# Optimization experiments

Hardware: AMD Instinct MI355X
Metric: run time of the kernel (lower is better)

Reference implementation:

```python
import jax, jax.numpy as jnp
import numpy as np

RANK = 16
ALPHA = 32
SCALING = ALPHA / RANK  # 2.0


def setup_inputs() -> dict:
    key = jax.random.key(0)
    k1, k2, k3 = jax.random.split(key, 3)
    B_, S, D, O = 2, 4096, 4096, 4096
    x = jax.random.normal(k1, (B_, S, D), dtype=jnp.float32)
    # Dequantized base weight, torch Linear layout [out, in]
    W_base = jax.random.normal(k2, (O, D), dtype=jnp.float32) * 0.02
    # kaiming_uniform-ish init for lora_A [rank, in]
    bound = float(np.sqrt(6.0 / (1 + 5) / D))
    A = jax.random.uniform(k3, (RANK, D), dtype=jnp.float32, minval=-bound, maxval=bound)
    # lora_B initialized to zeros [out, rank]
    Bm = jnp.zeros((O, RANK), dtype=jnp.float32)
    return {"x": x, "W_base": W_base, "A": A, "B": Bm}


def reference(x, W_base, A, B):
    # Y = x @ W_base^T + (x @ A^T) @ B^T * scaling   (dropout p=0 -> identity)
    base_out = jnp.einsum('bsd,od->bso', x, W_base)
    lora_mid = jnp.einsum('bsd,rd->bsr', x, A)        # [B,S,rank]
    lora_out = jnp.einsum('bsr,or->bso', lora_mid, B) # [B,S,out]
    return base_out + lora_out * SCALING
```

## Files before the change

kernel.cpp:

```cpp
#include <hip/hip_runtime.h>
#include <hip/hip_bf16.h>

typedef __attribute__((ext_vector_type(8)))  __bf16 bf16x8;
typedef __attribute__((ext_vector_type(4)))  float  f32x4;

__global__ __launch_bounds__(256) void preproc(
    const float* __restrict__ x, const float* __restrict__ A,
    const float* __restrict__ Wf,
    float* __restrict__ mid, __bf16* __restrict__ Xb, __bf16* __restrict__ Wbb,
    int K, int M, long nW8, int wBlocks)
{
    int tid = threadIdx.x;
    if ((int)blockIdx.x < wBlocks) {
        long i = (long)blockIdx.x * 256 + tid;
        long stride = (long)wBlocks * 256;
        for (; i < nW8; i += stride) {
            const f32x4* p = (const f32x4*)(Wf + i * 8);
            f32x4 a = p[0], b = p[1];
            bf16x8 o;
            o[0] = (__bf16)a[0]; o[1] = (__bf16)a[1];
            o[2] = (__bf16)a[2]; o[3] = (__bf16)a[3];
            o[4] = (__bf16)b[0]; o[5] = (__bf16)b[1];
            o[6] = (__bf16)b[2]; o[7] = (__bf16)b[3];
            *(bf16x8*)(Wbb + i * 8) = o;
        }
        return;
    }

    int m0 = ((int)blockIdx.x - wBlocks) * 4;
    float acc[4][16];
#pragma unroll
    for (int row = 0; row < 4; ++row)
#pragma unroll
        for (int r = 0; r < 16; ++r) acc[row][r] = 0.f;

    int iters = K / 2048;
    for (int it = 0; it < iters; ++it) {
        int k = it * 2048 + tid * 8;
        f32x4 xv[4][2];
#pragma unroll
        for (int row = 0; row < 4; ++row) {
            if (m0 + row < M) {
                const float* xr = x + (size_t)(m0 + row) * K;
                xv[row][0] = *(const f32x4*)(xr + k);
                xv[row][1] = *(const f32x4*)(xr + k + 4);
                bf16x8 o;
                o[0] = (__bf16)xv[row][0][0]; o[1] = (__bf16)xv[row][0][1];
                o[2] = (__bf16)xv[row][0][2]; o[3] = (__bf16)xv[row][0][3];
                o[4] = (__bf16)xv[row][1][0]; o[5] = (__bf16)xv[row][1][1];
                o[6] = (__bf16)xv[row][1][2]; o[7] = (__bf16)xv[row][1][3];
                *(bf16x8*)(Xb + (size_t)(m0 + row) * K + k) = o;
            } else {
                f32x4 z = {0.f,0.f,0.f,0.f};
                xv[row][0] = z; xv[row][1] = z;
            }
        }
#pragma unroll
        for (int r = 0; r < 16; ++r) {
            const f32x4* ap = (const f32x4*)(A + (size_t)r * K + k);
            f32x4 a0 = ap[0], a1 = ap[1];
#pragma unroll
            for (int row = 0; row < 4; ++row) {
                acc[row][r] += xv[row][0][0]*a0[0] + xv[row][0][1]*a0[1]
                             + xv[row][0][2]*a0[2] + xv[row][0][3]*a0[3]
                             + xv[row][1][0]*a1[0] + xv[row][1][1]*a1[1]
                             + xv[row][1][2]*a1[2] + xv[row][1][3]*a1[3];
            }
        }
    }

#pragma unroll
    for (int row = 0; row < 4; ++row)
#pragma unroll
        for (int r = 0; r < 16; ++r)
#pragma unroll
            for (int off = 32; off > 0; off >>= 1)
                acc[row][r] += __shfl_down(acc[row][r], off, 64);

    __shared__ float red[4][4][16];
    int lane = tid & 63, w = tid >> 6;
    if (lane == 0) {
#pragma unroll
        for (int row = 0; row < 4; ++row)
#pragma unroll
            for (int r = 0; r < 16; ++r) red[w][row][r] = acc[row][r];
    }
    __syncthreads();
    if (tid < 64) {
        int row = tid >> 4, r = tid & 15;
        if (m0 + row < M) {
            float s = red[0][row][r] + red[1][row][r]
                    + red[2][row][r] + red[3][row][r];
            mid[(size_t)(m0 + row) * 16 + r] = s;
        }
    }
}

__global__ __launch_bounds__(256) void mid_only(
    const float* __restrict__ x, const float* __restrict__ A,
    float* __restrict__ mid, int K, int M)
{
    int tid = threadIdx.x;
    int m0 = blockIdx.x * 4;
    float acc[4][16];
#pragma unroll
    for (int row = 0; row < 4; ++row)
#pragma unroll
        for (int r = 0; r < 16; ++r) acc[row][r] = 0.f;
    int iters = K / 2048;
    for (int it = 0; it < iters; ++it) {
        int k = it * 2048 + tid * 8;
        f32x4 xv[4][2];
#pragma unroll
        for (int row = 0; row < 4; ++row) {
            if (m0 + row < M) {
                const float* xr = x + (size_t)(m0 + row) * K;
                xv[row][0] = *(const f32x4*)(xr + k);
                xv[row][1] = *(const f32x4*)(xr + k + 4);
            } else {
                f32x4 z = {0.f,0.f,0.f,0.f};
                xv[row][0] = z; xv[row][1] = z;
            }
        }
#pragma unroll
        for (int r = 0; r < 16; ++r) {
            const f32x4* ap = (const f32x4*)(A + (size_t)r * K + k);
            f32x4 a0 = ap[0], a1 = ap[1];
#pragma unroll
            for (int row = 0; row < 4; ++row) {
                acc[row][r] += xv[row][0][0]*a0[0] + xv[row][0][1]*a0[1]
                             + xv[row][0][2]*a0[2] + xv[row][0][3]*a0[3]
                             + xv[row][1][0]*a1[0] + xv[row][1][1]*a1[1]
                             + xv[row][1][2]*a1[2] + xv[row][1][3]*a1[3];
            }
        }
    }
#pragma unroll
    for (int row = 0; row < 4; ++row)
#pragma unroll
        for (int r = 0; r < 16; ++r)
#pragma unroll
            for (int off = 32; off > 0; off >>= 1)
                acc[row][r] += __shfl_down(acc[row][r], off, 64);
    __shared__ float red[4][4][16];
    int lane = tid & 63, w = tid >> 6;
    if (lane == 0) {
#pragma unroll
        for (int row = 0; row < 4; ++row)
#pragma unroll
            for (int r = 0; r < 16; ++r) red[w][row][r] = acc[row][r];
    }
    __syncthreads();
    if (tid < 64) {
        int row = tid >> 4, r = tid & 15;
        if (m0 + row < M) {
            float s = red[0][row][r] + red[1][row][r]
                    + red[2][row][r] + red[3][row][r];
            mid[(size_t)(m0 + row) * 16 + r] = s;
        }
    }
}

#define GL16(g, l) __builtin_amdgcn_global_load_lds( \
    (const __attribute__((address_space(1))) void*)(g), \
    (__attribute__((address_space(3))) void*)(l), 16, 0, 0)

#define DSR(dst, addr, IMM) \
    asm volatile("ds_read_b128 %0, %1 offset:" IMM : "=v"(dst) : "v"(addr))

#define BAR()   __builtin_amdgcn_s_barrier()
#define LGKM0() asm volatile("s_waitcnt lgkmcnt(0)" ::: )
#define SCHED() __builtin_amdgcn_sched_barrier(0)
#define VMW(n)  asm volatile("s_waitcnt vmcnt(" #n ")" ::: "memory")

__global__ __launch_bounds__(512, 2) void gemm256(
    const __bf16* __restrict__ Xb,
    const __bf16* __restrict__ Wb,
    const float*  __restrict__ mid,
    const float*  __restrict__ Bl,
    float* __restrict__ out,
    int M, int N, int K)
{
    __shared__ __bf16 As[4][256 * 32];
    __shared__ __bf16 Bs[4][256 * 32];

    const int NT = K >> 5;

    int nbx = N >> 8, nby = M >> 8, nwg = nbx * nby;
    int bid = blockIdx.x, swz = bid;
    if ((nwg & 7) == 0) { int cpx = nwg >> 3; swz = (bid & 7) * cpx + (bid >> 3); }
    int by = swz / nbx, bx = swz % nbx;
    int m0 = by << 8, n0 = bx << 8;

    int tid = threadIdx.x;
    int lane = tid & 63;
    int w = tid >> 6;
    int wm = w >> 2, wn = w & 3;

    int q0 = tid >> 2;
    int c0 = tid & 3;
    int csrc = c0 ^ ((q0 >> 1) & 3);
    const __bf16* sA0 = Xb + (size_t)(m0 + q0) * K + csrc * 8;
    const __bf16* sA1 = sA0 + (size_t)128 * K;
    const __bf16* sB0 = Wb + (size_t)(n0 + q0) * K + csrc * 8;
    const __bf16* sB1 = sB0 + (size_t)128 * K;
    unsigned ldsw = (unsigned)w * 1024;

#define STAGE_A(t, b) do { size_t ko = (size_t)(t) * 32; \
    GL16(sA0 + ko, (char*)As[b] + ldsw); \
    GL16(sA1 + ko, (char*)As[b] + 8192 + ldsw); } while (0)
#define STAGE_B(t, b) do { size_t ko = (size_t)(t) * 32; \
    GL16(sB0 + ko, (char*)Bs[b] + ldsw); \
    GL16(sB1 + ko, (char*)Bs[b] + 8192 + ldsw); } while (0)

    int chunkSwz = (lane >> 4) ^ ((lane >> 1) & 3);
    unsigned aoff = (unsigned)((wm * 128 + (lane & 15)) * 64 + chunkSwz * 16);
    unsigned boff = (unsigned)((wn * 64  + (lane & 15)) * 64 + chunkSwz * 16);
    unsigned a_addr = (unsigned)(size_t)(__attribute__((address_space(3))) __bf16*)&As[0][0] + aoff;
    unsigned b_addr = (unsigned)(size_t)(__attribute__((address_space(3))) __bf16*)&Bs[0][0] + boff;

    f32x4 acc[8][4];
    {
        int kh = lane >> 4;
        bf16x8 bI[4];
#pragma unroll
        for (int j = 0; j < 4; ++j) {
            bf16x8 v = {};
            if (kh < 2) {
                int col = n0 + wn * 64 + j * 16 + (lane & 15);
                const f32x4* p = (const f32x4*)(Bl + (size_t)col * 16 + kh * 8);
                f32x4 v0 = p[0], v1 = p[1];
                v[0] = (__bf16)(2.0f * v0[0]); v[1] = (__bf16)(2.0f * v0[1]);
                v[2] = (__bf16)(2.0f * v0[2]); v[3] = (__bf16)(2.0f * v0[3]);
                v[4] = (__bf16)(2.0f * v1[0]); v[5] = (__bf16)(2.0f * v1[1]);
                v[6] = (__bf16)(2.0f * v1[2]); v[7] = (__bf16)(2.0f * v1[3]);
            }
            bI[j] = v;
        }
#pragma unroll
        for (int i = 0; i < 8; ++i) {
            bf16x8 aI = {};
            if (kh < 2) {
                int row = m0 + wm * 128 + i * 16 + (lane & 15);
                const f32x4* p = (const f32x4*)(mid + (size_t)row * 16 + kh * 8);
                f32x4 v0 = p[0], v1 = p[1];
                aI[0] = (__bf16)v0[0]; aI[1] = (__bf16)v0[1];
                aI[2] = (__bf16)v0[2]; aI[3] = (__bf16)v0[3];
                aI[4] = (__bf16)v1[0]; aI[5] = (__bf16)v1[1];
                aI[6] = (__bf16)v1[2]; aI[7] = (__bf16)v1[3];
            }
            f32x4 z = {0.f, 0.f, 0.f, 0.f};
#pragma unroll
            for (int j = 0; j < 4; ++j)
                acc[i][j] = __builtin_amdgcn_mfma_f32_16x16x32_bf16(aI, bI[j], z, 0, 0, 0);
        }
    }

    STAGE_A(0, 0); STAGE_B(0, 0);
    STAGE_A(1, 1); STAGE_B(1, 1);
    STAGE_A(2, 2); STAGE_B(2, 2);
    STAGE_A(3, 3); STAGE_B(3, 3);
    VMW(12);
    BAR();

    bf16x8 axf0, axf1, axf2, axf3, bxf0, bxf1, bxf2, bxf3;
    bf16x8 ayf0, ayf1, ayf2, ayf3, byf0, byf1, byf2, byf3;
    bf16x8 ax4, ax5, ax6, ax7, ay4, ay5, ay6, ay7;

    DSR(axf0, a_addr, "0");    DSR(axf1, a_addr, "1024");
    DSR(axf2, a_addr, "2048"); DSR(axf3, a_addr, "3072");
    DSR(bxf0, b_addr, "0");    DSR(bxf1, b_addr, "1024");
    DSR(bxf2, b_addr, "2048"); DSR(bxf3, b_addr, "3072");

    for (int t = 0; t < NT; t += 2) {
        unsigned aT0 = a_addr + ((unsigned)(t & 3) << 14);
        unsigned aT1 = a_addr + ((unsigned)((t + 1) & 3) << 14);
        unsigned bT1 = b_addr + ((unsigned)((t + 1) & 3) << 14);
        unsigned aT2 = a_addr + ((unsigned)((t + 2) & 3) << 14);
        unsigned bT2 = b_addr + ((unsigned)((t + 2) & 3) << 14);
        bool p2 = (t + 2) < NT;
        bool p3 = (t + 3) < NT;
        bool p4 = (t + 4) < NT;
        bool p5 = (t + 5) < NT;

        LGKM0();
        BAR();
        SCHED();
        DSR(ax4, aT0, "4096"); DSR(ax5, aT0, "5120");
        DSR(ax6, aT0, "6144"); DSR(ax7, aT0, "7168");
        SCHED();
        __builtin_amdgcn_s_setprio(1);
        acc[0][0] = __builtin_amdgcn_mfma_f32_16x16x32_bf16(axf0, bxf0, acc[0][0], 0, 0, 0);
        acc[0][1] = __builtin_amdgcn_mfma_f32_16x16x32_bf16(axf0, bxf1, acc[0][1], 0, 0, 0);
        acc[0][2] = __builtin_amdgcn_mfma_f32_16x16x32_bf16(axf0, bxf2, acc[0][2], 0, 0, 0);
        acc[0][3] = __builtin_amdgcn_mfma_f32_16x16x32_bf16(axf0, bxf3, acc[0][3], 0, 0, 0);
        acc[1][0] = __builtin_amdgcn_mfma_f32_16x16x32_bf16(axf1, bxf0, acc[1][0], 0, 0, 0);
        acc[1][1] = __builtin_amdgcn_mfma_f32_16x16x32_bf16(axf1, bxf1, acc[1][1], 0, 0, 0);
        acc[1][2] = __builtin_amdgcn_mfma_f32_16x16x32_bf16(axf1, bxf2, acc[1][2], 0, 0, 0);
        acc[1][3] = __builtin_amdgcn_mfma_f32_16x16x32_bf16(axf1, bxf3, acc[1][3], 0, 0, 0);
        acc[2][0] = __builtin_amdgcn_mfma_f32_16x16x32_bf16(axf2, bxf0, acc[2][0], 0, 0, 0);
        acc[2][1] = __builtin_amdgcn_mfma_f32_16x16x32_bf16(axf2, bxf1, acc[2][1], 0, 0, 0);
        acc[2][2] = __builtin_amdgcn_mfma_f32_16x16x32_bf16(axf2, bxf2, acc[2][2], 0, 0, 0);
        acc[2][3] = __builtin_amdgcn_mfma_f32_16x16x32_bf16(axf2, bxf3, acc[2][3], 0, 0, 0);
        acc[3][0] = __builtin_amdgcn_mfma_f32_16x16x32_bf16(axf3, bxf0, acc[3][0], 0, 0, 0);
        acc[3][1] = __builtin_amdgcn_mfma_f32_16x16x32_bf16(axf3, bxf1, acc[3][1], 0, 0, 0);
        acc[3][2] = __builtin_amdgcn_mfma_f32_16x16x32_bf16(axf3, bxf2, acc[3][2], 0, 0, 0);
        acc[3][3] = __builtin_amdgcn_mfma_f32_16x16x32_bf16(axf3, bxf3, acc[3][3], 0, 0, 0);
        __builtin_amdgcn_s_setprio(0);

        LGKM0();
        if (p3)      { VMW(8); }
        else if (p2) { VMW(4); }
        else         { VMW(0); }
        BAR();
        SCHED();
        DSR(ayf0, aT1, "0");    DSR(ayf1, aT1, "1024");
        DSR(ayf2, aT1, "2048"); DSR(ayf3, aT1, "3072");
        DSR(byf0, bT1, "0");    DSR(byf1, bT1, "1024");
        DSR(byf2, bT1, "2048"); DSR(byf3, bT1, "3072");
        if (p4) { STAGE_A(t + 4, t & 3); STAGE_B(t + 4, t & 3); }
        SCHED();
        __builtin_amdgcn_s_setprio(1);
        acc[4][0] = __builtin_amdgcn_mfma_f32_16x16x32_bf16(ax4, bxf0, acc[4][0], 0, 0, 0);
        acc[4][1] = __builtin_amdgcn_mfma_f32_16x16x32_bf16(ax4, bxf1, acc[4][1], 0, 0, 0);
        acc[4][2] = __builtin_amdgcn_mfma_f32_16x16x32_bf16(ax4, bxf2, acc[4][2], 0, 0, 0);
        acc[4][3] = __builtin_amdgcn_mfma_f32_16x16x32_bf16(ax4, bxf3, acc[4][3], 0, 0, 0);
        acc[5][0] = __builtin_amdgcn_mfma_f32_16x16x32_bf16(ax5, bxf0, acc[5][0], 0, 0, 0);
        acc[5][1] = __builtin_amdgcn_mfma_f32_16x16x32_bf16(ax5, bxf1, acc[5][1], 0, 0, 0);
        acc[5][2] = __builtin_amdgcn_mfma_f32_16x16x32_bf16(ax5, bxf2, acc[5][2], 0, 0, 0);
        acc[5][3] = __builtin_amdgcn_mfma_f32_16x16x32_bf16(ax5, bxf3, acc[5][3], 0, 0, 0);
        acc[6][0] = __builtin_amdgcn_mfma_f32_16x16x32_bf16(ax6, bxf0, acc[6][0], 0, 0, 0);
        acc[6][1] = __builtin_amdgcn_mfma_f32_16x16x32_bf16(ax6, bxf1, acc[6][1], 0, 0, 0);
        acc[6][2] = __builtin_amdgcn_mfma_f32_16x16x32_bf16(ax6, bxf2, acc[6][2], 0, 0, 0);
        acc[6][3] = __builtin_amdgcn_mfma_f32_16x16x32_bf16(ax6, bxf3, acc[6][3], 0, 0, 0);
        acc[7][0] = __builtin_amdgcn_mfma_f32_16x16x32_bf16(ax7, bxf0, acc[7][0], 0, 0, 0);
        acc[7][1] = __builtin_amdgcn_mfma_f32_16x16x32_bf16(ax7, bxf1, acc[7][1], 0, 0, 0);
        acc[7][2] = __builtin_amdgcn_mfma_f32_16x16x32_bf16(ax7, bxf2, acc[7][2], 0, 0, 0);
        acc[7][3] = __builtin_amdgcn_mfma_f32_16x16x32_bf16(ax7, bxf3, acc[7][3], 0, 0, 0);
        __builtin_amdgcn_s_setprio(0);

        LGKM0();
        BAR();
        SCHED();
        DSR(ay4, aT1, "4096"); DSR(ay5, aT1, "5120");
        DSR(ay6, aT1, "6144"); DSR(ay7, aT1, "7168");
        SCHED();
        __builtin_amdgcn_s_setprio(1);
        acc[0][0] = __builtin_amdgcn_mfma_f32_16x16x32_bf16(ayf0, byf0, acc[0][0], 0, 0, 0);
        acc[0][1] = __builtin_amdgcn_mfma_f32_16x16x32_bf16(ayf0, byf1, acc[0][1], 0, 0, 0);
        acc[0][2] = __builtin_amdgcn_mfma_f32_16x16x32_bf16(ayf0, byf2, acc[0][2], 0, 0, 0);
        acc[0][3] = __builtin_amdgcn_mfma_f32_16x16x32_bf16(ayf0, byf3, acc[0][3], 0, 0, 0);
        acc[1][0] = __builtin_amdgcn_mfma_f32_16x16x32_bf16(ayf1, byf0, acc[1][0], 0, 0, 0);
        acc[1][1] = __builtin_amdgcn_mfma_f32_16x16x32_bf16(ayf1, byf1, acc[1][1], 0, 0, 0);
        acc[1][2] = __builtin_amdgcn_mfma_f32_16x16x32_bf16(ayf1, byf2, acc[1][2], 0, 0, 0);
        acc[1][3] = __builtin_amdgcn_mfma_f32_16x16x32_bf16(ayf1, byf3, acc[1][3], 0, 0, 0);
        acc[2][0] = __builtin_amdgcn_mfma_f32_16x16x32_bf16(ayf2, byf0, acc[2][0], 0, 0, 0);
        acc[2][1] = __builtin_amdgcn_mfma_f32_16x16x32_bf16(ayf2, byf1, acc[2][1], 0, 0, 0);
        acc[2][2] = __builtin_amdgcn_mfma_f32_16x16x32_bf16(ayf2, byf2, acc[2][2], 0, 0, 0);
        acc[2][3] = __builtin_amdgcn_mfma_f32_16x16x32_bf16(ayf2, byf3, acc[2][3], 0, 0, 0);
        acc[3][0] = __builtin_amdgcn_mfma_f32_16x16x32_bf16(ayf3, byf0, acc[3][0], 0, 0, 0);
        acc[3][1] = __builtin_amdgcn_mfma_f32_16x16x32_bf16(ayf3, byf1, acc[3][1], 0, 0, 0);
        acc[3][2] = __builtin_amdgcn_mfma_f32_16x16x32_bf16(ayf3, byf2, acc[3][2], 0, 0, 0);
        acc[3][3] = __builtin_amdgcn_mfma_f32_16x16x32_bf16(ayf3, byf3, acc[3][3], 0, 0, 0);
        __builtin_amdgcn_s_setprio(0);

        LGKM0();
        if (p4)      { VMW(8); }
        else if (p3) { VMW(4); }
        else         { VMW(0); }
        BAR();
        SCHED();
        if (p2) {
            DSR(axf0, aT2, "0");    DSR(axf1, aT2, "1024");
            DSR(axf2, aT2, "2048"); DSR(axf3, aT2, "3072");
            DSR(bxf0, bT2, "0");    DSR(bxf1, bT2, "1024");
            DSR(bxf2, bT2, "2048"); DSR(bxf3, bT2, "3072");
        }
        if (p5) { STAGE_A(t + 5, (t + 1) & 3); STAGE_B(t + 5, (t + 1) & 3); }
        SCHED();
        __builtin_amdgcn_s_setprio(1);
        acc[4][0] = __builtin_amdgcn_mfma_f32_16x16x32_bf16(ay4, byf0, acc[4][0], 0, 0, 0);
        acc[4][1] = __builtin_amdgcn_mfma_f32_16x16x32_bf16(ay4, byf1, acc[4][1], 0, 0, 0);
        acc[4][2] = __builtin_amdgcn_mfma_f32_16x16x32_bf16(ay4, byf2, acc[4][2], 0, 0, 0);
        acc[4][3] = __builtin_amdgcn_mfma_f32_16x16x32_bf16(ay4, byf3, acc[4][3], 0, 0, 0);
        acc[5][0] = __builtin_amdgcn_mfma_f32_16x16x32_bf16(ay5, byf0, acc[5][0], 0, 0, 0);
        acc[5][1] = __builtin_amdgcn_mfma_f32_16x16x32_bf16(ay5, byf1, acc[5][1], 0, 0, 0);
        acc[5][2] = __builtin_amdgcn_mfma_f32_16x16x32_bf16(ay5, byf2, acc[5][2], 0, 0, 0);
        acc[5][3] = __builtin_amdgcn_mfma_f32_16x16x32_bf16(ay5, byf3, acc[5][3], 0, 0, 0);
        acc[6][0] = __builtin_amdgcn_mfma_f32_16x16x32_bf16(ay6, byf0, acc[6][0], 0, 0, 0);
        acc[6][1] = __builtin_amdgcn_mfma_f32_16x16x32_bf16(ay6, byf1, acc[6][1], 0, 0, 0);
        acc[6][2] = __builtin_amdgcn_mfma_f32_16x16x32_bf16(ay6, byf2, acc[6][2], 0, 0, 0);
        acc[6][3] = __builtin_amdgcn_mfma_f32_16x16x32_bf16(ay6, byf3, acc[6][3], 0, 0, 0);
        acc[7][0] = __builtin_amdgcn_mfma_f32_16x16x32_bf16(ay7, byf0, acc[7][0], 0, 0, 0);
        acc[7][1] = __builtin_amdgcn_mfma_f32_16x16x32_bf16(ay7, byf1, acc[7][1], 0, 0, 0);
        acc[7][2] = __builtin_amdgcn_mfma_f32_16x16x32_bf16(ay7, byf2, acc[7][2], 0, 0, 0);
        acc[7][3] = __builtin_amdgcn_mfma_f32_16x16x32_bf16(ay7, byf3, acc[7][3], 0, 0, 0);
        __builtin_amdgcn_s_setprio(0);
    }

#pragma unroll
    for (int i = 0; i < 8; ++i) {
        int rbase = m0 + wm * 128 + i * 16 + ((lane >> 4) << 2);
#pragma unroll
        for (int q = 0; q < 4; ++q) {
            float* orow = out + (size_t)(rbase + q) * N;
            int colb = n0 + wn * 64 + (lane & 15);
            orow[colb]      = acc[i][0][q];
            orow[colb + 16] = acc[i][1][q];
            orow[colb + 32] = acc[i][2][q];
            orow[colb + 48] = acc[i][3][q];
        }
    }
}

__global__ __launch_bounds__(256) void gemm_fb(
    const float* __restrict__ X, const float* __restrict__ W,
    const float* __restrict__ mid, const float* __restrict__ Bl,
    float* __restrict__ out, int M, int N, int K)
{
    __shared__ float As[64][16];
    __shared__ float Bs[64][16];
    int nbx = N / 64;
    int bx = blockIdx.x % nbx, by = blockIdx.x / nbx;
    int m0 = by * 64, n0 = bx * 64;
    int tid = threadIdx.x;
    int tr = tid >> 4, tc = tid & 15;

    float acc[4][4] = {};
    for (int kt = 0; kt < K; kt += 16) {
#pragma unroll
        for (int s = 0; s < 4; ++s) {
            int c = s * 256 + tid;
            int row = c >> 4, kk = c & 15;
            As[row][kk] = X[(size_t)(m0 + row) * K + kt + kk];
            Bs[row][kk] = W[(size_t)(n0 + row) * K + kt + kk];
        }
        __syncthreads();
#pragma unroll
        for (int kk = 0; kk < 16; ++kk) {
            float av[4], bv[4];
#pragma unroll
            for (int i = 0; i < 4; ++i) { av[i] = As[tr*4+i][kk]; bv[i] = Bs[tc*4+i][kk]; }
#pragma unroll
            for (int i = 0; i < 4; ++i)
#pragma unroll
                for (int j = 0; j < 4; ++j) acc[i][j] += av[i] * bv[j];
        }
        __syncthreads();
    }
#pragma unroll
    for (int i = 0; i < 4; ++i) {
        int row = m0 + tr * 4 + i;
#pragma unroll
        for (int j = 0; j < 4; ++j) {
            int col = n0 + tc * 4 + j;
            float s = 0.f;
#pragma unroll
            for (int r = 0; r < 16; ++r)
                s += mid[(size_t)row * 16 + r] * Bl[(size_t)col * 16 + r];
            out[(size_t)row * N + col] = acc[i][j] + 2.0f * s;
        }
    }
}

extern "C" void kernel_launch(void* const* d_in, const int* in_sizes, int n_in,
                              void* d_out, int out_size, void* d_ws, size_t ws_size,
                              hipStream_t stream)
{
    const float* x   = (const float*)d_in[0];
    const float* Wf  = (const float*)d_in[1];
    const float* A   = (const float*)d_in[2];
    const float* Bl  = (const float*)d_in[3];
    float* out = (float*)d_out;

    int D = in_sizes[2] / 16;
    int O = in_sizes[3] / 16;
    long M = (long)in_sizes[0] / D;
    int K = D, N = O;

    size_t xb_bytes  = (size_t)M * K * 2;
    size_t wb_bytes  = (size_t)N * K * 2;
    size_t mid_bytes = (size_t)M * 16 * 4;

    bool shapes_ok = (M % 256 == 0) && (N % 256 == 0) && (K % 2048 == 0)
                     && (K / 32 >= 8);

    int midBlocks = (int)((M + 3) / 4);

    if (shapes_ok && ws_size >= xb_bytes + wb_bytes + mid_bytes) {
        __bf16* Xb  = (__bf16*)d_ws;
        __bf16* Wbb = (__bf16*)((char*)d_ws + xb_bytes);
        float*  mid = (float*)((char*)d_ws + xb_bytes + wb_bytes);

        const int wBlocks = 1024;
        long nW8 = (long)N * K / 8;
        preproc<<<wBlocks + midBlocks, 256, 0, stream>>>(
            x, A, Wf, mid, Xb, Wbb, K, (int)M, nW8, wBlocks);
        int nwg = (int)(M / 256) * (N / 256);
        gemm256<<<nwg, 512, 0, stream>>>(Xb, Wbb, mid, Bl, out, (int)M, N, K);
    } else {
        float* mid = (float*)d_ws;
        mid_only<<<midBlocks, 256, 0, stream>>>(x, A, mid, K, (int)M);
        int nwg = (int)(M / 64) * (N / 64);
        gemm_fb<<<nwg, 256, 0, stream>>>(x, Wf, mid, Bl, out, (int)M, N, K);
    }
}
```

Before: 330.6 us.

## Restructure GEMM main loop to two-stage prefetch with split A/B staging

Replaces the 4-deep global-to-LDS prefetch and register double-buffered fragment loads with a simpler per-tile loop. It prefetches only 2 tiles ahead and issues the A stage and B stage in separate halves of the iteration. LDS fragment reads are no longer overlapped with the previous MFMA block; each half reads its fragments, waits, then computes. The intent is to cut register pressure and scheduling complexity, at the cost of less latency hiding and an extra barrier per half-step.

```diff
diff --git a/kernel.cpp b/kernel.cpp
--- a/kernel.cpp
+++ b/kernel.cpp
@@ -170,7 +170,7 @@
 
 #define BAR()   __builtin_amdgcn_s_barrier()
 #define LGKM0() asm volatile("s_waitcnt lgkmcnt(0)" ::: )
-#define SCHED() __builtin_amdgcn_sched_barrier(0)
+#define FENCE() __builtin_amdgcn_sched_barrier(0)
 #define VMW(n)  asm volatile("s_waitcnt vmcnt(" #n ")" ::: "memory")
 
 __global__ __launch_bounds__(512, 2) void gemm256(
@@ -258,144 +258,74 @@
 
     STAGE_A(0, 0); STAGE_B(0, 0);
     STAGE_A(1, 1); STAGE_B(1, 1);
-    STAGE_A(2, 2); STAGE_B(2, 2);
-    STAGE_A(3, 3); STAGE_B(3, 3);
-    VMW(12);
+    VMW(4);
     BAR();
 
-    bf16x8 axf0, axf1, axf2, axf3, bxf0, bxf1, bxf2, bxf3;
-    bf16x8 ayf0, ayf1, ayf2, ayf3, byf0, byf1, byf2, byf3;
-    bf16x8 ax4, ax5, ax6, ax7, ay4, ay5, ay6, ay7;
-
-    DSR(axf0, a_addr, "0");    DSR(axf1, a_addr, "1024");
-    DSR(axf2, a_addr, "2048"); DSR(axf3, a_addr, "3072");
-    DSR(bxf0, b_addr, "0");    DSR(bxf1, b_addr, "1024");
-    DSR(bxf2, b_addr, "2048"); DSR(bxf3, b_addr, "3072");
-
-    for (int t = 0; t < NT; t += 2) {
-        unsigned aT0 = a_addr + ((unsigned)(t & 3) << 14);
-        unsigned aT1 = a_addr + ((unsigned)((t + 1) & 3) << 14);
-        unsigned bT1 = b_addr + ((unsigned)((t + 1) & 3) << 14);
-        unsigned aT2 = a_addr + ((unsigned)((t + 2) & 3) << 14);
-        unsigned bT2 = b_addr + ((unsigned)((t + 2) & 3) << 14);
+    bf16x8 af0, af1, af2, af3, af4, af5, af6, af7, bf0, bf1, bf2, bf3;
+
+    for (int t = 0; t < NT; ++t) {
+        unsigned aT = a_addr + ((unsigned)(t & 3) << 14);
+        unsigned bT = b_addr + ((unsigned)(t & 3) << 14);
         bool p2 = (t + 2) < NT;
-        bool p3 = (t + 3) < NT;
-        bool p4 = (t + 4) < NT;
-        bool p5 = (t + 5) < NT;
-
+
+        DSR(bf0, bT, "0");    DSR(bf1, bT, "1024");
+        DSR(bf2, bT, "2048"); DSR(bf3, bT, "3072");
+        DSR(af0, aT, "0");    DSR(af1, aT, "1024");
+        DSR(af2, aT, "2048"); DSR(af3, aT, "3072");
+        if (p2) STAGE_A(t + 2, (t + 2) & 3);
+        BAR();
         LGKM0();
+        FENCE();
+        __builtin_amdgcn_s_setprio(1);
+        acc[0][0] = __builtin_amdgcn_mfma_f32_16x16x32_bf16(af0, bf0, acc[0][0], 0, 0, 0);
+        acc[0][1] = __builtin_amdgcn_mfma_f32_16x16x32_bf16(af0, bf1, acc[0][1], 0, 0, 0);
+        acc[0][2] = __builtin_amdgcn_mfma_f32_16x16x32_bf16(af0, bf2, acc[0][2], 0, 0, 0);
+        acc[0][3] = __builtin_amdgcn_mfma_f32_16x16x32_bf16(af0, bf3, acc[0][3], 0, 0, 0);
+        acc[1][0] = __builtin_amdgcn_mfma_f32_16x16x32_bf16(af1, bf0, acc[1][0], 0, 0, 0);
+        acc[1][1] = __builtin_amdgcn_mfma_f32_16x16x32_bf16(af1, bf1, acc[1][1], 0, 0, 0);
+        acc[1][2] = __builtin_amdgcn_mfma_f32_16x16x32_bf16(af1, bf2, acc[1][2], 0, 0, 0);
+        acc[1][3] = __builtin_amdgcn_mfma_f32_16x16x32_bf16(af1, bf3, acc[1][3], 0, 0, 0);
+        acc[2][0] = __builtin_amdgcn_mfma_f32_16x16x32_bf16(af2, bf0, acc[2][0], 0, 0, 0);
+        acc[2][1] = __builtin_amdgcn_mfma_f32_16x16x32_bf16(af2, bf1, acc[2][1], 0, 0, 0);
+        acc[2][2] = __builtin_amdgcn_mfma_f32_16x16x32_bf16(af2, bf2, acc[2][2], 0, 0, 0);
+        acc[2][3] = __builtin_amdgcn_mfma_f32_16x16x32_bf16(af2, bf3, acc[2][3], 0, 0, 0);
+        acc[3][0] = __builtin_amdgcn_mfma_f32_16x16x32_bf16(af3, bf0, acc[3][0], 0, 0, 0);
+        acc[3][1] = __builtin_amdgcn_mfma_f32_16x16x32_bf16(af3, bf1, acc[3][1], 0, 0, 0);
+        acc[3][2] = __builtin_amdgcn_mfma_f32_16x16x32_bf16(af3, bf2, acc[3][2], 0, 0, 0);
+        acc[3][3] = __builtin_amdgcn_mfma_f32_16x16x32_bf16(af3, bf3, acc[3][3], 0, 0, 0);
+        __builtin_amdgcn_s_setprio(0);
         BAR();
-        SCHED();
-        DSR(ax4, aT0, "4096"); DSR(ax5, aT0, "5120");
-        DSR(ax6, aT0, "6144"); DSR(ax7, aT0, "7168");
-        SCHED();
+
+        DSR(af4, aT, "4096"); DSR(af5, aT, "5120");
+        DSR(af6, aT, "6144"); DSR(af7, aT, "7168");
+        if (p2) {
+            STAGE_B(t + 2, (t + 2) & 3);
+            VMW(4);
+        } else {
+            VMW(0);
+        }
+        BAR();
+        LGKM0();
+        FENCE();
         __builtin_amdgcn_s_setprio(1);
-        acc[0][0] = __builtin_amdgcn_mfma_f32_16x16x32_bf16(axf0, bxf0, acc[0][0], 0, 0, 0);
-        acc[0][1] = __builtin_amdgcn_mfma_f32_16x16x32_bf16(axf0, bxf1, acc[0][1], 0, 0, 0);
-        acc[0][2] = __builtin_amdgcn_mfma_f32_16x16x32_bf16(axf0, bxf2, acc[0][2], 0, 0, 0);
-        acc[0][3] = __builtin_amdgcn_mfma_f32_16x16x32_bf16(axf0, bxf3, acc[0][3], 0, 0, 0);
-        acc[1][0] = __builtin_amdgcn_mfma_f32_16x16x32_bf16(axf1, bxf0, acc[1][0], 0, 0, 0);
-        acc[1][1] = __builtin_amdgcn_mfma_f32_16x16x32_bf16(axf1, bxf1, acc[1][1], 0, 0, 0);
-        acc[1][2] = __builtin_amdgcn_mfma_f32_16x16x32_bf16(axf1, bxf2, acc[1][2], 0, 0, 0);
-        acc[1][3] = __builtin_amdgcn_mfma_f32_16x16x32_bf16(axf1, bxf3, acc[1][3], 0, 0, 0);
-        acc[2][0] = __builtin_amdgcn_mfma_f32_16x16x32_bf16(axf2, bxf0, acc[2][0], 0, 0, 0);
-        acc[2][1] = __builtin_amdgcn_mfma_f32_16x16x32_bf16(axf2, bxf1, acc[2][1], 0, 0, 0);
-        acc[2][2] = __builtin_amdgcn_mfma_f32_16x16x32_bf16(axf2, bxf2, acc[2][2], 0, 0, 0);
-        acc[2][3] = __builtin_amdgcn_mfma_f32_16x16x32_bf16(axf2, bxf3, acc[2][3], 0, 0, 0);
-        acc[3][0] = __builtin_amdgcn_mfma_f32_16x16x32_bf16(axf3, bxf0, acc[3][0], 0, 0, 0);
-        acc[3][1] = __builtin_amdgcn_mfma_f32_16x16x32_bf16(axf3, bxf1, acc[3][1], 0, 0, 0);
-        acc[3][2] = __builtin_amdgcn_mfma_f32_16x16x32_bf16(axf3, bxf2, acc[3][2], 0, 0, 0);
-        acc[3][3] = __builtin_amdgcn_mfma_f32_16x16x32_bf16(axf3, bxf3, acc[3][3], 0, 0, 0);
+        acc[4][0] = __builtin_amdgcn_mfma_f32_16x16x32_bf16(af4, bf0, acc[4][0], 0, 0, 0);
+        acc[4][1] = __builtin_amdgcn_mfma_f32_16x16x32_bf16(af4, bf1, acc[4][1], 0, 0, 0);
+        acc[4][2] = __builtin_amdgcn_mfma_f32_16x16x32_bf16(af4, bf2, acc[4][2], 0, 0, 0);
+        acc[4][3] = __builtin_amdgcn_mfma_f32_16x16x32_bf16(af4, bf3, acc[4][3], 0, 0, 0);
+        acc[5][0] = __builtin_amdgcn_mfma_f32_16x16x32_bf16(af5, bf0, acc[5][0], 0, 0, 0);
+        acc[5][1] = __builtin_amdgcn_mfma_f32_16x16x32_bf16(af5, bf1, acc[5][1], 0, 0, 0);
+        acc[5][2] = __builtin_amdgcn_mfma_f32_16x16x32_bf16(af5, bf2, acc[5][2], 0, 0, 0);
+        acc[5][3] = __builtin_amdgcn_mfma_f32_16x16x32_bf16(af5, bf3, acc[5][3], 0, 0, 0);
+        acc[6][0] = __builtin_amdgcn_mfma_f32_16x16x32_bf16(af6, bf0, acc[6][0], 0, 0, 0);
+        acc[6][1] = __builtin_amdgcn_mfma_f32_16x16x32_bf16(af6, bf1, acc[6][1], 0, 0, 0);
+        acc[6][2] = __builtin_amdgcn_mfma_f32_16x16x32_bf16(af6, bf2, acc[6][2], 0, 0, 0);
+        acc[6][3] = __builtin_amdgcn_mfma_f32_16x16x32_bf16(af6, bf3, acc[6][3], 0, 0, 0);
+        acc[7][0] = __builtin_amdgcn_mfma_f32_16x16x32_bf16(af7, bf0, acc[7][0], 0, 0, 0);
+        acc[7][1] = __builtin_amdgcn_mfma_f32_16x16x32_bf16(af7, bf1, acc[7][1], 0, 0, 0);
+        acc[7][2] = __builtin_amdgcn_mfma_f32_16x16x32_bf16(af7, bf2, acc[7][2], 0, 0, 0);
+        acc[7][3] = __builtin_amdgcn_mfma_f32_16x16x32_bf16(af7, bf3, acc[7][3], 0, 0, 0);
         __builtin_amdgcn_s_setprio(0);
-
-        LGKM0();
-        if (p3)      { VMW(8); }
-        else if (p2) { VMW(4); }
-        else         { VMW(0); }
         BAR();
-        SCHED();
-        DSR(ayf0, aT1, "0");    DSR(ayf1, aT1, "1024");
-        DSR(ayf2, aT1, "2048"); DSR(ayf3, aT1, "3072");
-        DSR(byf0, bT1, "0");    DSR(byf1, bT1, "1024");
-        DSR(byf2, bT1, "2048"); DSR(byf3, bT1, "3072");
-        if (p4) { STAGE_A(t + 4, t & 3); STAGE_B(t + 4, t & 3); }
-        SCHED();
-        __builtin_amdgcn_s_setprio(1);
-        acc[4][0] = __builtin_amdgcn_mfma_f32_16x16x32_bf16(ax4, bxf0, acc[4][0], 0, 0, 0);
-        acc[4][1] = __builtin_amdgcn_mfma_f32_16x16x32_bf16(ax4, bxf1, acc[4][1], 0, 0, 0);
-        acc[4][2] = __builtin_amdgcn_mfma_f32_16x16x32_bf16(ax4, bxf2, acc[4][2], 0, 0, 0);
-        acc[4][3] = __builtin_amdgcn_mfma_f32_16x16x32_bf16(ax4, bxf3, acc[4][3], 0, 0, 0);
-        acc[5][0] = __builtin_amdgcn_mfma_f32_16x16x32_bf16(ax5, bxf0, acc[5][0], 0, 0, 0);
-        acc[5][1] = __builtin_amdgcn_mfma_f32_16x16x32_bf16(ax5, bxf1, acc[5][1], 0, 0, 0);
-        acc[5][2] = __builtin_amdgcn_mfma_f32_16x16x32_bf16(ax5, bxf2, acc[5][2], 0, 0, 0);
-        acc[5][3] = __builtin_amdgcn_mfma_f32_16x16x32_bf16(ax5, bxf3, acc[5][3], 0, 0, 0);
-        acc[6][0] = __builtin_amdgcn_mfma_f32_16x16x32_bf16(ax6, bxf0, acc[6][0], 0, 0, 0);
-        acc[6][1] = __builtin_amdgcn_mfma_f32_16x16x32_bf16(ax6, bxf1, acc[6][1], 0, 0, 0);
-        acc[6][2] = __builtin_amdgcn_mfma_f32_16x16x32_bf16(ax6, bxf2, acc[6][2], 0, 0, 0);
-        acc[6][3] = __builtin_amdgcn_mfma_f32_16x16x32_bf16(ax6, bxf3, acc[6][3], 0, 0, 0);
-        acc[7][0] = __builtin_amdgcn_mfma_f32_16x16x32_bf16(ax7, bxf0, acc[7][0], 0, 0, 0);
-        acc[7][1] = __builtin_amdgcn_mfma_f32_16x16x32_bf16(ax7, bxf1, acc[7][1], 0, 0, 0);
-        acc[7][2] = __builtin_amdgcn_mfma_f32_16x16x32_bf16(ax7, bxf2, acc[7][2], 0, 0, 0);
-        acc[7][3] = __builtin_amdgcn_mfma_f32_16x16x32_bf16(ax7, bxf3, acc[7][3], 0, 0, 0);
-        __builtin_amdgcn_s_setprio(0);
-
-        LGKM0();
-        BAR();
-        SCHED();
-        DSR(ay4, aT1, "4096"); DSR(ay5, aT1, "5120");
-        DSR(ay6, aT1, "6144"); DSR(ay7, aT1, "7168");
-        SCHED();
-        __builtin_amdgcn_s_setprio(1);
-        acc[0][0] = __builtin_amdgcn_mfma_f32_16x16x32_bf16(ayf0, byf0, acc[0][0], 0, 0, 0);
-        acc[0][1] = __builtin_amdgcn_mfma_f32_16x16x32_bf16(ayf0, byf1, acc[0][1], 0, 0, 0);
-        acc[0][2] = __builtin_amdgcn_mfma_f32_16x16x32_bf16(ayf0, byf2, acc[0][2], 0, 0, 0);
-        acc[0][3] = __builtin_amdgcn_mfma_f32_16x16x32_bf16(ayf0, byf3, acc[0][3], 0, 0, 0);
-        acc[1][0] = __builtin_amdgcn_mfma_f32_16x16x32_bf16(ayf1, byf0, acc[1][0], 0, 0, 0);
-        acc[1][1] = __builtin_amdgcn_mfma_f32_16x16x32_bf16(ayf1, byf1, acc[1][1], 0, 0, 0);
-        acc[1][2] = __builtin_amdgcn_mfma_f32_16x16x32_bf16(ayf1, byf2, acc[1][2], 0, 0, 0);
-        acc[1][3] = __builtin_amdgcn_mfma_f32_16x16x32_bf16(ayf1, byf3, acc[1][3], 0, 0, 0);
-        acc[2][0] = __builtin_amdgcn_mfma_f32_16x16x32_bf16(ayf2, byf0, acc[2][0], 0, 0, 0);
-        acc[2][1] = __builtin_amdgcn_mfma_f32_16x16x32_bf16(ayf2, byf1, acc[2][1], 0, 0, 0);
-        acc[2][2] = __builtin_amdgcn_mfma_f32_16x16x32_bf16(ayf2, byf2, acc[2][2], 0, 0, 0);
-        acc[2][3] = __builtin_amdgcn_mfma_f32_16x16x32_bf16(ayf2, byf3, acc[2][3], 0, 0, 0);
-        acc[3][0] = __builtin_amdgcn_mfma_f32_16x16x32_bf16(ayf3, byf0, acc[3][0], 0, 0, 0);
-        acc[3][1] = __builtin_amdgcn_mfma_f32_16x16x32_bf16(ayf3, byf1, acc[3][1], 0, 0, 0);
-        acc[3][2] = __builtin_amdgcn_mfma_f32_16x16x32_bf16(ayf3, byf2, acc[3][2], 0, 0, 0);
-        acc[3][3] = __builtin_amdgcn_mfma_f32_16x16x32_bf16(ayf3, byf3, acc[3][3], 0, 0, 0);
-        __builtin_amdgcn_s_setprio(0);
-
-        LGKM0();
-        if (p4)      { VMW(8); }
-        else if (p3) { VMW(4); }
-        else         { VMW(0); }
-        BAR();
-        SCHED();
-        if (p2) {
-            DSR(axf0, aT2, "0");    DSR(axf1, aT2, "1024");
-            DSR(axf2, aT2, "2048"); DSR(axf3, aT2, "3072");
-            DSR(bxf0, bT2, "0");    DSR(bxf1, bT2, "1024");
-            DSR(bxf2, bT2, "2048"); DSR(bxf3, bT2, "3072");
-        }
-        if (p5) { STAGE_A(t + 5, (t + 1) & 3); STAGE_B(t + 5, (t + 1) & 3); }
-        SCHED();
-        __builtin_amdgcn_s_setprio(1);
-        acc[4][0] = __builtin_amdgcn_mfma_f32_16x16x32_bf16(ay4, byf0, acc[4][0], 0, 0, 0);
-        acc[4][1] = __builtin_amdgcn_mfma_f32_16x16x32_bf16(ay4, byf1, acc[4][1], 0, 0, 0);
-        acc[4][2] = __builtin_amdgcn_mfma_f32_16x16x32_bf16(ay4, byf2, acc[4][2], 0, 0, 0);
-        acc[4][3] = __builtin_amdgcn_mfma_f32_16x16x32_bf16(ay4, byf3, acc[4][3], 0, 0, 0);
-        acc[5][0] = __builtin_amdgcn_mfma_f32_16x16x32_bf16(ay5, byf0, acc[5][0], 0, 0, 0);
-        acc[5][1] = __builtin_amdgcn_mfma_f32_16x16x32_bf16(ay5, byf1, acc[5][1], 0, 0, 0);
-        acc[5][2] = __builtin_amdgcn_mfma_f32_16x16x32_bf16(ay5, byf2, acc[5][2], 0, 0, 0);
-        acc[5][3] = __builtin_amdgcn_mfma_f32_16x16x32_bf16(ay5, byf3, acc[5][3], 0, 0, 0);
-        acc[6][0] = __builtin_amdgcn_mfma_f32_16x16x32_bf16(ay6, byf0, acc[6][0], 0, 0, 0);
-        acc[6][1] = __builtin_amdgcn_mfma_f32_16x16x32_bf16(ay6, byf1, acc[6][1], 0, 0, 0);
-        acc[6][2] = __builtin_amdgcn_mfma_f32_16x16x32_bf16(ay6, byf2, acc[6][2], 0, 0, 0);
-        acc[6][3] = __builtin_amdgcn_mfma_f32_16x16x32_bf16(ay6, byf3, acc[6][3], 0, 0, 0);
-        acc[7][0] = __builtin_amdgcn_mfma_f32_16x16x32_bf16(ay7, byf0, acc[7][0], 0, 0, 0);
-        acc[7][1] = __builtin_amdgcn_mfma_f32_16x16x32_bf16(ay7, byf1, acc[7][1], 0, 0, 0);
-        acc[7][2] = __builtin_amdgcn_mfma_f32_16x16x32_bf16(ay7, byf2, acc[7][2], 0, 0, 0);
-        acc[7][3] = __builtin_amdgcn_mfma_f32_16x16x32_bf16(ay7, byf3, acc[7][3], 0, 0, 0);
-        __builtin_amdgcn_s_setprio(0);
     }
 
 #pragma unroll
```

New measurement: 338.5 us. 2.4% more time.
